# Performance work log

Hardware: AMD Instinct MI355X
Metric: run time of the kernel (lower is better)

## Reference

```python
import jax, jax.numpy as jnp
import numpy as np

N = 50000   # vertices
E = 25000   # hyperedges
NNZ = 400000  # incidence pairs (v, e)
D_IN = 512
D_OUT = 512  # heads * out_channels, heads=1


def setup_inputs() -> dict:
    key = jax.random.key(0)
    kx, kw, kv, ke = jax.random.split(key, 4)
    X = jax.random.normal(kx, (N, D_IN), dtype=jnp.float32)
    W = jax.random.normal(kw, (D_OUT, D_IN), dtype=jnp.float32) * 0.02  # nn.Linear weight [out,in]
    vidx = jax.random.randint(kv, (NNZ,), 0, N, dtype=jnp.int32)
    eidx = jax.random.randint(ke, (NNZ,), 0, E, dtype=jnp.int32)
    # degE = 1/|e| (hyperedge size), degV = 1/deg(v), as precomputed by hyperg
    ones = jnp.ones((NNZ,), dtype=jnp.float32)
    edge_sz = jax.ops.segment_sum(ones, eidx, num_segments=E)
    vert_dg = jax.ops.segment_sum(ones, vidx, num_segments=N)
    degE = 1.0 / jnp.maximum(edge_sz, 1.0)
    degV = 1.0 / jnp.maximum(vert_dg, 1.0)
    Wdiag = jnp.ones((E,), dtype=jnp.float32)
    return {"X": X, "W": W, "degE": degE, "degV": degV, "Wdiag": Wdiag,
            "vidx": vidx, "eidx": eidx}


def reference(X, W, degE, degV, Wdiag, vidx, eidx):
    # Dense projection: X @ W^T (nn.Linear, no bias)
    Xp = jnp.einsum('nd,od->no', X, W)                      # [N, D_OUT]
    # Stage 1: vertex -> hyperedge (first_aggr: mean via degE), weighted by Wdiag
    Xe = jax.ops.segment_sum(Xp[vidx], eidx, num_segments=E)  # [E, D_OUT]
    Xe = Xe * (degE * Wdiag)[:, None]
    # Stage 2: hyperedge -> vertex, normalized by degV
    Xv = jax.ops.segment_sum(Xe[eidx], vidx, num_segments=N)  # [N, D_OUT]
    Xv = Xv * degV[:, None]
    return Xv
```

## Files before the change

kernel.cpp:

```cpp
#include <hip/hip_runtime.h>

typedef unsigned short u16;
typedef unsigned int   u32;
typedef __attribute__((ext_vector_type(4))) float f32x4;
typedef __attribute__((ext_vector_type(4))) u32   u32x4;
typedef __attribute__((ext_vector_type(4))) int   i32x4;
typedef __attribute__((ext_vector_type(8))) __bf16 bf16x8;

constexpr int NV   = 50000;
constexpr int NE   = 25000;
constexpr int NNZp = 400000;
constexpr int D    = 512;
constexpr int MP2  = 25088;
constexpr int NBE  = 25;
constexpr int NBV  = 49;
constexpr int BPS1 = 391;
constexpr int BPS2 = 1563;

static __device__ __forceinline__ u16 f2bf(float f) {
  u32 u = __float_as_uint(f);
  u32 r = (u + 0x7fffu + ((u >> 16) & 1u)) >> 16;
  return (u16)r;
}
static __device__ __forceinline__ u32 pk2(float a, float b) {
  return (u32)f2bf(a) | ((u32)f2bf(b) << 16);
}

static __device__ __forceinline__ void gload_lds16(const u16* g, u16* l) {
  __builtin_amdgcn_global_load_lds(
      (const __attribute__((address_space(1))) u32*)g,
      (__attribute__((address_space(3))) u32*)l, 16, 0, 0);
}

__global__ void zero_kernel(int* cntE, int* cntV, int* dhistE, int* dhistV) {
  int i = blockIdx.x * 256 + threadIdx.x;
  if (i < NE) cntE[i] = 0;
  if (i < NV) cntV[i] = 0;
  if (i < 64) { dhistE[i] = 0; dhistV[i] = 0; }
}

__global__ void hist_kernel(const int* __restrict__ vidx, const int* __restrict__ eidx,
                            int* cntE, int* cntV) {
  int i = blockIdx.x * 256 + threadIdx.x;
  if (i < NNZp) {
    atomicAdd(&cntE[eidx[i]], 1);
    atomicAdd(&cntV[vidx[i]], 1);
  }
}

__global__ __launch_bounds__(256) void deghist_kernel(
    const int* __restrict__ cntE, const int* __restrict__ cntV, int* dhistE, int* dhistV) {
  __shared__ int lhE[64], lhV[64];
  int t = threadIdx.x;
  if (t < 64) { lhE[t] = 0; lhV[t] = 0; }
  __syncthreads();
  int i = blockIdx.x * 256 + t;
  if (i < NE) atomicAdd(&lhE[min(cntE[i], 63)], 1);
  if (i < NV) atomicAdd(&lhV[min(cntV[i], 63)], 1);
  __syncthreads();
  if (t < 64) { if (lhE[t]) atomicAdd(&dhistE[t], lhE[t]); }
  else if (t < 128) { int u = t - 64; if (lhV[u]) atomicAdd(&dhistV[u], lhV[u]); }
}

__global__ __launch_bounds__(256) void scan1_kernel(
    const int* __restrict__ cntE, const int* __restrict__ cntV,
    int* offE, int* offV, int* blkSum) {
  const bool isE = blockIdx.x < NBE;
  const int* cnt = isE ? cntE : cntV;
  int* off = isE ? offE : offV;
  const int len = isE ? NE : NV;
  const int t = threadIdx.x;
  const int base = (isE ? blockIdx.x : blockIdx.x - NBE) * 1024 + t * 4;
  int4 c = {0, 0, 0, 0};
  if (base + 4 <= len) c = *(const int4*)(cnt + base);
  else {
    if (base + 0 < len) c.x = cnt[base + 0];
    if (base + 1 < len) c.y = cnt[base + 1];
    if (base + 2 < len) c.z = cnt[base + 2];
    if (base + 3 < len) c.w = cnt[base + 3];
  }
  int s = c.x + c.y + c.z + c.w;
  __shared__ int sm[256];
  sm[t] = s;
  __syncthreads();
  for (int d = 1; d < 256; d <<= 1) {
    int u = (t >= d) ? sm[t - d] : 0;
    __syncthreads();
    sm[t] += u;
    __syncthreads();
  }
  int ex = sm[t] - s;
  int4 o;
  o.x = ex; o.y = o.x + c.x; o.z = o.y + c.y; o.w = o.z + c.z;
  if (base + 4 <= len) *(int4*)(off + base) = o;
  else {
    if (base + 0 < len) off[base + 0] = o.x;
    if (base + 1 < len) off[base + 1] = o.y;
    if (base + 2 < len) off[base + 2] = o.z;
    if (base + 3 < len) off[base + 3] = o.w;
  }
  if (t == 255) blkSum[blockIdx.x] = sm[255];
}

__global__ void scan2_kernel(int* blkSum, const int* __restrict__ dhistE,
                             const int* __restrict__ dhistV, int* dcurE, int* dcurV) {
  int wv = threadIdx.x >> 6, lane = threadIdx.x & 63;
  const int* s; int* d; int len;
  if (wv == 0)      { s = blkSum;       d = blkSum;       len = NBE; }
  else if (wv == 1) { s = blkSum + NBE; d = blkSum + NBE; len = NBV; }
  else if (wv == 2) { s = dhistE;       d = dcurE;        len = 64;  }
  else              { s = dhistV;       d = dcurV;        len = 64;  }
  int v = (lane < len) ? s[lane] : 0;
  int incl = v;
#pragma unroll
  for (int dd = 1; dd < 64; dd <<= 1) {
    int u = __shfl_up(incl, dd, 64);
    if (lane >= dd) incl += u;
  }
  if (lane < len) d[lane] = incl - v;
}

__global__ __launch_bounds__(256) void scan3_kernel(
    int* offE, int* offV, int* curE, int* curV, const int* __restrict__ blkSum) {
  const bool isE = blockIdx.x < NBE;
  int* off = isE ? offE : offV;
  int* cur = isE ? curE : curV;
  const int len = isE ? NE : NV;
  const int pref = blkSum[blockIdx.x];
  const int base = (isE ? blockIdx.x : blockIdx.x - NBE) * 1024 + threadIdx.x * 4;
  if (base + 4 <= len) {
    int4 o = *(int4*)(off + base);
    o.x += pref; o.y += pref; o.z += pref; o.w += pref;
    *(int4*)(off + base) = o;
    *(int4*)(cur + base) = o;
  } else {
    for (int q = 0; q < 4; q++)
      if (base + q < len) { int v = off[base + q] + pref; off[base + q] = v; cur[base + q] = v; }
  }
}

__global__ void scatter_kernel(const int* __restrict__ vidx, const int* __restrict__ eidx,
                               int* curE, int* curV, int* csr_ev, int* csr_ve) {
  int i = blockIdx.x * 256 + threadIdx.x;
  if (i < NNZp) {
    int e = eidx[i], v = vidx[i];
    csr_ev[atomicAdd(&curE[e], 1)] = v;
    csr_ve[atomicAdd(&curV[v], 1)] = e;
  }
}

__global__ __launch_bounds__(256) void degsort_kernel(
    const int* __restrict__ cntE, const int* __restrict__ offE,
    const int* __restrict__ cntV, const int* __restrict__ offV,
    const float* __restrict__ degV, int* dcurE, int* dcurV,
    i32x4* sE_meta, i32x4* sV_meta) {
  __shared__ int lhE[64], lhV[64], lbE[64], lbV[64];
  int t = threadIdx.x;
  if (t < 64) { lhE[t] = 0; lhV[t] = 0; }
  __syncthreads();
  int i = blockIdx.x * 256 + t;
  int bE = 0, rE = 0, bV = 0, rV = 0;
  if (i < NE) { bE = min(cntE[i], 63); rE = atomicAdd(&lhE[bE], 1); }
  if (i < NV) { bV = min(cntV[i], 63); rV = atomicAdd(&lhV[bV], 1); }
  __syncthreads();
  if (t < 64) { lbE[t] = lhE[t] ? atomicAdd(&dcurE[t], lhE[t]) : 0; }
  else if (t < 128) { int u = t - 64; lbV[u] = lhV[u] ? atomicAdd(&dcurV[u], lhV[u]) : 0; }
  __syncthreads();
  if (i < NE) {
    int r = lbE[bE] + rE;
    i32x4 m = { i, offE[i], cntE[i], 0 };
    sE_meta[r] = m;
  }
  if (i < NV) {
    int r = lbV[bV] + rV;
    i32x4 m = { i, offV[i], cntV[i], __float_as_int(degV[i]) };
    sV_meta[r] = m;
  }
}

__global__ __launch_bounds__(256) void convert_kernel(
    const float* __restrict__ X, const float* __restrict__ W,
    u16* __restrict__ Xb, u16* __restrict__ Wb) {
  constexpr size_t NX = (size_t)NV * D;
  size_t i = ((size_t)blockIdx.x * 256 + threadIdx.x) * 8;
  const float* src;
  u16* dst;
  if (i < NX) {
    int n = (int)(i >> 9);
    int col = (int)(i & 511);
    int t = col >> 5, w = col & 31;
    src = X + i;
    dst = Xb + (size_t)t * NV * 32 + (size_t)n * 32 + w;
  } else {
    src = W + (i - NX);
    dst = Wb + (i - NX);
  }
  f32x4 a = *(const f32x4*)src;
  f32x4 b = *(const f32x4*)(src + 4);
  u32x4 p = { pk2(a[0], a[1]), pk2(a[2], a[3]), pk2(b[0], b[1]), pk2(b[2], b[3]) };
  __builtin_nontemporal_store(p, (u32x4*)dst);
}

__global__ __launch_bounds__(256) void stage1_kernel(
    const u16* __restrict__ Xb, const i32x4* __restrict__ sE_meta,
    const int* __restrict__ csr_ev, u16* __restrict__ XeR) {
  const int wave = threadIdx.x >> 6;
  const int lane = threadIdx.x & 63;
  const int g    = lane >> 2;
  const int c    = lane & 3;
  const int bid  = blockIdx.x;
  const int xcd  = bid & 7;
  const int tmp  = bid >> 3;
  const int phase = (tmp >= BPS1) ? 1 : 0;
  const int eg    = tmp - phase * BPS1;
  const int t     = xcd + 8 * phase;
  const int rank  = eg * 64 + wave * 16 + g;
  const u16* base = Xb + (size_t)t * NV * 32;
  int e = 0, start = 0, cnt = 0;
  if (rank < NE) {
    i32x4 m = __builtin_nontemporal_load(sE_meta + rank);
    e = m.x; start = m.y; cnt = m.z;
  }
  float acc[8] = {};
  int b0 = 0;
  for (; b0 + 16 <= cnt; b0 += 16) {
    int idx[16];
#pragma unroll
    for (int p = 0; p < 16; p++) idx[p] = __builtin_nontemporal_load(csr_ev + start + b0 + p);
    u32x4 pk[16];
#pragma unroll
    for (int p = 0; p < 16; p++) pk[p] = *(const u32x4*)(base + (size_t)idx[p] * 32 + c * 8);
#pragma unroll
    for (int p = 0; p < 16; p++)
#pragma unroll
      for (int q = 0; q < 4; q++) {
        u32 u = pk[p][q];
        acc[2 * q]     += __uint_as_float(u << 16);
        acc[2 * q + 1] += __uint_as_float(u & 0xffff0000u);
      }
  }
  const int rem = cnt - b0;
  if (rem > 0) {
    int idx[16];
#pragma unroll
    for (int p = 0; p < 16; p++) {
      int j = __builtin_nontemporal_load(csr_ev + start + b0 + p);
      idx[p] = (p < rem) ? j : 0;
    }
    u32x4 pk[16];
#pragma unroll
    for (int p = 0; p < 16; p++) pk[p] = *(const u32x4*)(base + (size_t)idx[p] * 32 + c * 8);
#pragma unroll
    for (int p = 0; p < 16; p++)
      if (p < rem)
#pragma unroll
        for (int q = 0; q < 4; q++) {
          u32 u = pk[p][q];
          acc[2 * q]     += __uint_as_float(u << 16);
          acc[2 * q + 1] += __uint_as_float(u & 0xffff0000u);
        }
  }
  if (rank < NE) {
    u32x4 o = { pk2(acc[0], acc[1]), pk2(acc[2], acc[3]),
                pk2(acc[4], acc[5]), pk2(acc[6], acc[7]) };
    __builtin_nontemporal_store(o, (u32x4*)(XeR + (size_t)e * D + t * 32 + c * 8));
  }
}

__global__ __launch_bounds__(256) void gemm_kernel(const u16* __restrict__ A,
                                                   const u16* __restrict__ B,
                                                   const float* __restrict__ degE,
                                                   const float* __restrict__ Wdiag,
                                                   u16* __restrict__ C) {
  __shared__ u16 sA[128 * 32];
  __shared__ u16 sB[128 * 32];
  const int tid  = threadIdx.x;
  const int lane = tid & 63;
  const int wave = tid >> 6;
  const int bm = blockIdx.y * 128;
  const int bn = blockIdx.x * 128;
  const int wm = (wave >> 1) * 64;
  const int wn = (wave & 1) * 64;
  const int lr = lane & 15;
  const int lk = (lane >> 4) * 8;
  const int srow = lane >> 2;
  const int scol = (lane & 3) * 8;

  f32x4 acc[4][4] = {};

  for (int kt = 0; kt < D; kt += 32) {
    __syncthreads();
#pragma unroll
    for (int c = 0; c < 2; c++) {
      const int ar = wave * 16 + c * 64;
      gload_lds16(A + (size_t)(bm + ar + srow) * D + kt + scol, &sA[ar * 32]);
      gload_lds16(B + (size_t)(bn + ar + srow) * D + kt + scol, &sB[ar * 32]);
    }
    __syncthreads();

    bf16x8 af[4], bfr[4];
#pragma unroll
    for (int i = 0; i < 4; i++) af[i]  = *(const bf16x8*)&sA[(wm + i * 16 + lr) * 32 + lk];
#pragma unroll
    for (int j = 0; j < 4; j++) bfr[j] = *(const bf16x8*)&sB[(wn + j * 16 + lr) * 32 + lk];
#pragma unroll
    for (int i = 0; i < 4; i++)
#pragma unroll
      for (int j = 0; j < 4; j++)
        acc[i][j] = __builtin_amdgcn_mfma_f32_16x16x32_bf16(af[i], bfr[j], acc[i][j], 0, 0, 0);
  }

#pragma unroll
  for (int i = 0; i < 4; i++)
#pragma unroll
    for (int r = 0; r < 4; r++) {
      int row = bm + wm + i * 16 + (lane >> 4) * 4 + r;
      if (row < NE) {
        float se = degE[row] * Wdiag[row];
#pragma unroll
        for (int j = 0; j < 4; j++) {
          int col = bn + wn + lr + j * 16;
          int s = col >> 6, w = col & 63;
          __builtin_nontemporal_store(f2bf(acc[i][j][r] * se),
                                      C + (size_t)s * MP2 * 64 + (size_t)row * 64 + w);
        }
      }
    }
}

__global__ __launch_bounds__(256) void stage2_kernel(
    const u16* __restrict__ Xe2, const i32x4* __restrict__ sV_meta,
    const int* __restrict__ csr_ve, float* __restrict__ out) {
  const int wave = threadIdx.x >> 6;
  const int lane = threadIdx.x & 63;
  const int g    = lane >> 3;
  const int c    = lane & 7;
  const int s    = blockIdx.x & 7;
  const int vg   = blockIdx.x >> 3;
  const int rank = vg * 32 + wave * 8 + g;
  const u16* base = Xe2 + (size_t)s * MP2 * 64;
  int v = 0, start = 0, cnt = 0;
  float dv = 0.f;
  if (rank < NV) {
    i32x4 m = __builtin_nontemporal_load(sV_meta + rank);
    v = m.x; start = m.y; cnt = m.z; dv = __int_as_float(m.w);
  }
  float acc[8] = {};
  int b0 = 0;
  for (; b0 + 16 <= cnt; b0 += 16) {
    int idx[16];
#pragma unroll
    for (int p = 0; p < 16; p++) idx[p] = __builtin_nontemporal_load(csr_ve + start + b0 + p);
    u32x4 pk[16];
#pragma unroll
    for (int p = 0; p < 16; p++) pk[p] = *(const u32x4*)(base + (size_t)idx[p] * 64 + c * 8);
#pragma unroll
    for (int p = 0; p < 16; p++)
#pragma unroll
      for (int q = 0; q < 4; q++) {
        u32 u = pk[p][q];
        acc[2 * q]     += __uint_as_float(u << 16);
        acc[2 * q + 1] += __uint_as_float(u & 0xffff0000u);
      }
  }
  const int rem = cnt - b0;
  if (rem > 0) {
    int idx[16];
#pragma unroll
    for (int p = 0; p < 16; p++) {
      int j = __builtin_nontemporal_load(csr_ve + start + b0 + p);
      idx[p] = (p < rem) ? j : 0;
    }
    u32x4 pk[16];
#pragma unroll
    for (int p = 0; p < 16; p++) pk[p] = *(const u32x4*)(base + (size_t)idx[p] * 64 + c * 8);
#pragma unroll
    for (int p = 0; p < 16; p++)
      if (p < rem)
#pragma unroll
        for (int q = 0; q < 4; q++) {
          u32 u = pk[p][q];
          acc[2 * q]     += __uint_as_float(u << 16);
          acc[2 * q + 1] += __uint_as_float(u & 0xffff0000u);
        }
  }
  if (rank < NV) {
    float* orow = out + (size_t)v * D + s * 64 + c * 8;
    f32x4 o0 = { acc[0] * dv, acc[1] * dv, acc[2] * dv, acc[3] * dv };
    f32x4 o1 = { acc[4] * dv, acc[5] * dv, acc[6] * dv, acc[7] * dv };
    __builtin_nontemporal_store(o0, (f32x4*)orow);
    __builtin_nontemporal_store(o1, (f32x4*)(orow + 4));
  }
}

extern "C" void kernel_launch(void* const* d_in, const int* in_sizes, int n_in,
                              void* d_out, int out_size, void* d_ws, size_t ws_size,
                              hipStream_t stream) {
  const float* X     = (const float*)d_in[0];
  const float* W     = (const float*)d_in[1];
  const float* degE  = (const float*)d_in[2];
  const float* degV  = (const float*)d_in[3];
  const float* Wdiag = (const float*)d_in[4];
  const int*   vidx  = (const int*)d_in[5];
  const int*   eidx  = (const int*)d_in[6];
  float* out = (float*)d_out;

  char* p = (char*)d_ws;
  auto take = [&](size_t bytes) { char* r = p; p += (bytes + 255) & ~(size_t)255; return r; };
  u16* Xb     = (u16*)take((size_t)NV * D * 2);
  u16* Wb     = (u16*)take((size_t)D * D * 2);
  u16* XeR    = (u16*)take((size_t)MP2 * D * 2);
  u16* Xe2    = (u16*)take((size_t)MP2 * D * 2);
  int* cntE   = (int*)take((size_t)NE * 4);
  int* offE   = (int*)take((size_t)NE * 4);
  int* curE   = (int*)take((size_t)NE * 4);
  int* cntV   = (int*)take((size_t)NV * 4);
  int* offV   = (int*)take((size_t)NV * 4);
  int* curV   = (int*)take((size_t)NV * 4);
  int* csr_ev = (int*)take((size_t)NNZp * 4);
  int* csr_ve = (int*)take((size_t)NNZp * 4);
  int* blkSum = (int*)take((size_t)(NBE + NBV) * 4);
  int* dhistE = (int*)take(64 * 4);
  int* dhistV = (int*)take(64 * 4);
  int* dcurE  = (int*)take(64 * 4);
  int* dcurV  = (int*)take(64 * 4);
  i32x4* sE_meta = (i32x4*)take((size_t)NE * 16);
  i32x4* sV_meta = (i32x4*)take((size_t)NV * 16);

  constexpr size_t NCONV = ((size_t)NV * D + (size_t)D * D) / 8 / 256;
  constexpr int NSEG = (NV + 255) / 256;

  zero_kernel   <<<NSEG, 256, 0, stream>>>(cntE, cntV, dhistE, dhistV);
  hist_kernel   <<<(NNZp + 255) / 256, 256, 0, stream>>>(vidx, eidx, cntE, cntV);
  deghist_kernel<<<NSEG, 256, 0, stream>>>(cntE, cntV, dhistE, dhistV);
  scan1_kernel  <<<NBE + NBV, 256, 0, stream>>>(cntE, cntV, offE, offV, blkSum);
  scan2_kernel  <<<1, 256, 0, stream>>>(blkSum, dhistE, dhistV, dcurE, dcurV);
  scan3_kernel  <<<NBE + NBV, 256, 0, stream>>>(offE, offV, curE, curV, blkSum);
  scatter_kernel<<<(NNZp + 255) / 256, 256, 0, stream>>>(vidx, eidx, curE, curV, csr_ev, csr_ve);
  degsort_kernel<<<NSEG, 256, 0, stream>>>(cntE, offE, cntV, offV, degV, dcurE, dcurV,
                                           sE_meta, sV_meta);
  convert_kernel<<<NCONV, 256, 0, stream>>>(X, W, Xb, Wb);
  stage1_kernel <<<BPS1 * 16, 256, 0, stream>>>(Xb, sE_meta, csr_ev, XeR);
  gemm_kernel   <<<dim3(D / 128, MP2 / 128), 256, 0, stream>>>(XeR, Wb, degE, Wdiag, Xe2);
  stage2_kernel <<<BPS2 * 8, 256, 0, stream>>>(Xe2, sV_meta, csr_ve, out);
}
```

Before: 527.1 us.

## Share gather indices via lane shuffles and drop nontemporal hints

The two gather kernels stop having every lane load all 16 indices of a batch. Each lane group now loads its indices cooperatively, one or two per lane, and broadcasts them with __shfl, in batches of 8 with per-element bounds checks. This replaces the 16-wide unrolled main loop and its separate remainder path. All nontemporal loads and stores become ordinary loads and stores, so written intermediates can stay in cache for the next kernel. The trade-off is less memory-level parallelism per iteration, since 8 gathers are in flight instead of 16, plus extra shuffle and branch overhead.

```diff
diff --git a/kernel.cpp b/kernel.cpp
--- a/kernel.cpp
+++ b/kernel.cpp
@@ -198,7 +198,7 @@
   f32x4 a = *(const f32x4*)src;
   f32x4 b = *(const f32x4*)(src + 4);
   u32x4 p = { pk2(a[0], a[1]), pk2(a[2], a[3]), pk2(b[0], b[1]), pk2(b[2], b[3]) };
-  __builtin_nontemporal_store(p, (u32x4*)dst);
+  *(u32x4*)dst = p;
 }
 
 __global__ __launch_bounds__(256) void stage1_kernel(
@@ -218,52 +218,38 @@
   const u16* base = Xb + (size_t)t * NV * 32;
   int e = 0, start = 0, cnt = 0;
   if (rank < NE) {
-    i32x4 m = __builtin_nontemporal_load(sE_meta + rank);
+    i32x4 m = sE_meta[rank];
     e = m.x; start = m.y; cnt = m.z;
   }
   float acc[8] = {};
-  int b0 = 0;
-  for (; b0 + 16 <= cnt; b0 += 16) {
-    int idx[16];
-#pragma unroll
-    for (int p = 0; p < 16; p++) idx[p] = __builtin_nontemporal_load(csr_ev + start + b0 + p);
-    u32x4 pk[16];
-#pragma unroll
-    for (int p = 0; p < 16; p++) pk[p] = *(const u32x4*)(base + (size_t)idx[p] * 32 + c * 8);
-#pragma unroll
-    for (int p = 0; p < 16; p++)
-#pragma unroll
-      for (int q = 0; q < 4; q++) {
-        u32 u = pk[p][q];
-        acc[2 * q]     += __uint_as_float(u << 16);
-        acc[2 * q + 1] += __uint_as_float(u & 0xffff0000u);
+  for (int j0 = 0; j0 < cnt; j0 += 8) {
+    int i0 = 0, i1 = 0;
+    if (j0 + c < cnt)     i0 = csr_ev[start + j0 + c];
+    if (j0 + 4 + c < cnt) i1 = csr_ev[start + j0 + 4 + c];
+    u32x4 pk[8];
+#pragma unroll
+    for (int k = 0; k < 8; k++) {
+      if (j0 + k < cnt) {
+        int v = __shfl((k < 4) ? i0 : i1, (lane & ~3) | (k & 3), 64);
+        pk[k] = *(const u32x4*)(base + (size_t)v * 32 + c * 8);
       }
-  }
-  const int rem = cnt - b0;
-  if (rem > 0) {
-    int idx[16];
-#pragma unroll
-    for (int p = 0; p < 16; p++) {
-      int j = __builtin_nontemporal_load(csr_ev + start + b0 + p);
-      idx[p] = (p < rem) ? j : 0;
-    }
-    u32x4 pk[16];
-#pragma unroll
-    for (int p = 0; p < 16; p++) pk[p] = *(const u32x4*)(base + (size_t)idx[p] * 32 + c * 8);
-#pragma unroll
-    for (int p = 0; p < 16; p++)
-      if (p < rem)
+    }
+#pragma unroll
+    for (int k = 0; k < 8; k++) {
+      if (j0 + k < cnt) {
 #pragma unroll
         for (int q = 0; q < 4; q++) {
-          u32 u = pk[p][q];
+          u32 u = pk[k][q];
           acc[2 * q]     += __uint_as_float(u << 16);
           acc[2 * q + 1] += __uint_as_float(u & 0xffff0000u);
         }
+      }
+    }
   }
   if (rank < NE) {
     u32x4 o = { pk2(acc[0], acc[1]), pk2(acc[2], acc[3]),
                 pk2(acc[4], acc[5]), pk2(acc[6], acc[7]) };
-    __builtin_nontemporal_store(o, (u32x4*)(XeR + (size_t)e * D + t * 32 + c * 8));
+    *(u32x4*)(XeR + (size_t)e * D + t * 32 + c * 8) = o;
   }
 }
 
@@ -321,8 +307,7 @@
         for (int j = 0; j < 4; j++) {
           int col = bn + wn + lr + j * 16;
           int s = col >> 6, w = col & 63;
-          __builtin_nontemporal_store(f2bf(acc[i][j][r] * se),
-                                      C + (size_t)s * MP2 * 64 + (size_t)row * 64 + w);
+          C[(size_t)s * MP2 * 64 + (size_t)row * 64 + w] = f2bf(acc[i][j][r] * se);
         }
       }
     }
@@ -342,54 +327,39 @@
   int v = 0, start = 0, cnt = 0;
   float dv = 0.f;
   if (rank < NV) {
-    i32x4 m = __builtin_nontemporal_load(sV_meta + rank);
+    i32x4 m = sV_meta[rank];
     v = m.x; start = m.y; cnt = m.z; dv = __int_as_float(m.w);
   }
   float acc[8] = {};
-  int b0 = 0;
-  for (; b0 + 16 <= cnt; b0 += 16) {
-    int idx[16];
-#pragma unroll
-    for (int p = 0; p < 16; p++) idx[p] = __builtin_nontemporal_load(csr_ve + start + b0 + p);
-    u32x4 pk[16];
-#pragma unroll
-    for (int p = 0; p < 16; p++) pk[p] = *(const u32x4*)(base + (size_t)idx[p] * 64 + c * 8);
-#pragma unroll
-    for (int p = 0; p < 16; p++)
-#pragma unroll
-      for (int q = 0; q < 4; q++) {
-        u32 u = pk[p][q];
-        acc[2 * q]     += __uint_as_float(u << 16);
-        acc[2 * q + 1] += __uint_as_float(u & 0xffff0000u);
+  for (int j0 = 0; j0 < cnt; j0 += 8) {
+    int i0 = 0;
+    if (j0 + c < cnt) i0 = csr_ve[start + j0 + c];
+    u32x4 pk[8];
+#pragma unroll
+    for (int k = 0; k < 8; k++) {
+      if (j0 + k < cnt) {
+        int e = __shfl(i0, (lane & ~7) | k, 64);
+        pk[k] = *(const u32x4*)(base + (size_t)e * 64 + c * 8);
       }
-  }
-  const int rem = cnt - b0;
-  if (rem > 0) {
-    int idx[16];
-#pragma unroll
-    for (int p = 0; p < 16; p++) {
-      int j = __builtin_nontemporal_load(csr_ve + start + b0 + p);
-      idx[p] = (p < rem) ? j : 0;
-    }
-    u32x4 pk[16];
-#pragma unroll
-    for (int p = 0; p < 16; p++) pk[p] = *(const u32x4*)(base + (size_t)idx[p] * 64 + c * 8);
-#pragma unroll
-    for (int p = 0; p < 16; p++)
-      if (p < rem)
+    }
+#pragma unroll
+    for (int k = 0; k < 8; k++) {
+      if (j0 + k < cnt) {
 #pragma unroll
         for (int q = 0; q < 4; q++) {
-          u32 u = pk[p][q];
+          u32 u = pk[k][q];
           acc[2 * q]     += __uint_as_float(u << 16);
           acc[2 * q + 1] += __uint_as_float(u & 0xffff0000u);
         }
+      }
+    }
   }
   if (rank < NV) {
     float* orow = out + (size_t)v * D + s * 64 + c * 8;
     f32x4 o0 = { acc[0] * dv, acc[1] * dv, acc[2] * dv, acc[3] * dv };
     f32x4 o1 = { acc[4] * dv, acc[5] * dv, acc[6] * dv, acc[7] * dv };
-    __builtin_nontemporal_store(o0, (f32x4*)orow);
-    __builtin_nontemporal_store(o1, (f32x4*)(orow + 4));
+    *(f32x4*)orow = o0;
+    *(f32x4*)(orow + 4) = o1;
   }
 }
 
```

Measured after the change: 422.3 us. 1.25x faster.

## Fuse degree histogram and degree sort into scan kernels, shuffle-distribute gather indices

Applied to the files above, without the earlier changes.

Removes the separate deghist and degsort kernels by folding the degree histogram into scan1 and the bucketed meta placement into scan3, cutting two launches and extra passes over the count arrays. In stage1 and stage2 the lanes of each group now load distinct CSR indices and broadcast them with wave shuffles, instead of every lane loading all 16 indices. Nontemporal loads on meta and index arrays become plain loads. Degree-sorted order within a bucket changes, which only affects scheduling.

```diff
diff --git a/kernel.cpp b/kernel.cpp
--- a/kernel.cpp
+++ b/kernel.cpp
@@ -48,26 +48,13 @@
   }
 }
 
-__global__ __launch_bounds__(256) void deghist_kernel(
-    const int* __restrict__ cntE, const int* __restrict__ cntV, int* dhistE, int* dhistV) {
-  __shared__ int lhE[64], lhV[64];
-  int t = threadIdx.x;
-  if (t < 64) { lhE[t] = 0; lhV[t] = 0; }
-  __syncthreads();
-  int i = blockIdx.x * 256 + t;
-  if (i < NE) atomicAdd(&lhE[min(cntE[i], 63)], 1);
-  if (i < NV) atomicAdd(&lhV[min(cntV[i], 63)], 1);
-  __syncthreads();
-  if (t < 64) { if (lhE[t]) atomicAdd(&dhistE[t], lhE[t]); }
-  else if (t < 128) { int u = t - 64; if (lhV[u]) atomicAdd(&dhistV[u], lhV[u]); }
-}
-
 __global__ __launch_bounds__(256) void scan1_kernel(
     const int* __restrict__ cntE, const int* __restrict__ cntV,
-    int* offE, int* offV, int* blkSum) {
+    int* offE, int* offV, int* blkSum, int* dhistE, int* dhistV) {
   const bool isE = blockIdx.x < NBE;
   const int* cnt = isE ? cntE : cntV;
   int* off = isE ? offE : offV;
+  int* dhist = isE ? dhistE : dhistV;
   const int len = isE ? NE : NV;
   const int t = threadIdx.x;
   const int base = (isE ? blockIdx.x : blockIdx.x - NBE) * 1024 + t * 4;
@@ -81,8 +68,14 @@
   }
   int s = c.x + c.y + c.z + c.w;
   __shared__ int sm[256];
+  __shared__ int lh[64];
+  if (t < 64) lh[t] = 0;
   sm[t] = s;
   __syncthreads();
+  if (base + 0 < len) atomicAdd(&lh[min(c.x, 63)], 1);
+  if (base + 1 < len) atomicAdd(&lh[min(c.y, 63)], 1);
+  if (base + 2 < len) atomicAdd(&lh[min(c.z, 63)], 1);
+  if (base + 3 < len) atomicAdd(&lh[min(c.w, 63)], 1);
   for (int d = 1; d < 256; d <<= 1) {
     int u = (t >= d) ? sm[t - d] : 0;
     __syncthreads();
@@ -100,6 +93,7 @@
     if (base + 3 < len) off[base + 3] = o.w;
   }
   if (t == 255) blkSum[blockIdx.x] = sm[255];
+  if (t < 64 && lh[t]) atomicAdd(&dhist[t], lh[t]);
 }
 
 __global__ void scan2_kernel(int* blkSum, const int* __restrict__ dhistE,
@@ -121,22 +115,57 @@
 }
 
 __global__ __launch_bounds__(256) void scan3_kernel(
-    int* offE, int* offV, int* curE, int* curV, const int* __restrict__ blkSum) {
+    int* offE, int* offV, int* curE, int* curV, const int* __restrict__ blkSum,
+    const int* __restrict__ cntE, const int* __restrict__ cntV,
+    const float* __restrict__ degV, int* dcurE, int* dcurV,
+    i32x4* sE_meta, i32x4* sV_meta) {
   const bool isE = blockIdx.x < NBE;
   int* off = isE ? offE : offV;
   int* cur = isE ? curE : curV;
+  const int* cnt = isE ? cntE : cntV;
+  int* dcur = isE ? dcurE : dcurV;
+  i32x4* meta = isE ? sE_meta : sV_meta;
   const int len = isE ? NE : NV;
   const int pref = blkSum[blockIdx.x];
-  const int base = (isE ? blockIdx.x : blockIdx.x - NBE) * 1024 + threadIdx.x * 4;
+  const int t = threadIdx.x;
+  const int base = (isE ? blockIdx.x : blockIdx.x - NBE) * 1024 + t * 4;
+  __shared__ int lh[64], lb[64];
+  if (t < 64) lh[t] = 0;
+  __syncthreads();
+  int os[4] = {}, cs[4] = {};
+  bool val[4] = {};
   if (base + 4 <= len) {
     int4 o = *(int4*)(off + base);
-    o.x += pref; o.y += pref; o.z += pref; o.w += pref;
-    *(int4*)(off + base) = o;
-    *(int4*)(cur + base) = o;
+    int4 c = *(const int4*)(cnt + base);
+    os[0] = o.x + pref; os[1] = o.y + pref; os[2] = o.z + pref; os[3] = o.w + pref;
+    cs[0] = c.x; cs[1] = c.y; cs[2] = c.z; cs[3] = c.w;
+    val[0] = val[1] = val[2] = val[3] = true;
+    int4 oo = {os[0], os[1], os[2], os[3]};
+    *(int4*)(off + base) = oo;
+    *(int4*)(cur + base) = oo;
   } else {
     for (int q = 0; q < 4; q++)
-      if (base + q < len) { int v = off[base + q] + pref; off[base + q] = v; cur[base + q] = v; }
-  }
+      if (base + q < len) {
+        os[q] = off[base + q] + pref; cs[q] = cnt[base + q]; val[q] = true;
+        off[base + q] = os[q]; cur[base + q] = os[q];
+      }
+  }
+  int bq[4] = {}, rk[4] = {};
+#pragma unroll
+  for (int q = 0; q < 4; q++)
+    if (val[q]) { bq[q] = min(cs[q], 63); rk[q] = atomicAdd(&lh[bq[q]], 1); }
+  __syncthreads();
+  if (t < 64) lb[t] = lh[t] ? atomicAdd(&dcur[t], lh[t]) : 0;
+  __syncthreads();
+#pragma unroll
+  for (int q = 0; q < 4; q++)
+    if (val[q]) {
+      int id = base + q;
+      int dw = 0;
+      if (!isE) dw = __float_as_int(degV[id]);
+      i32x4 m = { id, os[q], cs[q], dw };
+      meta[lb[bq[q]] + rk[q]] = m;
+    }
 }
 
 __global__ void scatter_kernel(const int* __restrict__ vidx, const int* __restrict__ eidx,
@@ -146,35 +175,6 @@
     int e = eidx[i], v = vidx[i];
     csr_ev[atomicAdd(&curE[e], 1)] = v;
     csr_ve[atomicAdd(&curV[v], 1)] = e;
-  }
-}
-
-__global__ __launch_bounds__(256) void degsort_kernel(
-    const int* __restrict__ cntE, const int* __restrict__ offE,
-    const int* __restrict__ cntV, const int* __restrict__ offV,
-    const float* __restrict__ degV, int* dcurE, int* dcurV,
-    i32x4* sE_meta, i32x4* sV_meta) {
-  __shared__ int lhE[64], lhV[64], lbE[64], lbV[64];
-  int t = threadIdx.x;
-  if (t < 64) { lhE[t] = 0; lhV[t] = 0; }
-  __syncthreads();
-  int i = blockIdx.x * 256 + t;
-  int bE = 0, rE = 0, bV = 0, rV = 0;
-  if (i < NE) { bE = min(cntE[i], 63); rE = atomicAdd(&lhE[bE], 1); }
-  if (i < NV) { bV = min(cntV[i], 63); rV = atomicAdd(&lhV[bV], 1); }
-  __syncthreads();
-  if (t < 64) { lbE[t] = lhE[t] ? atomicAdd(&dcurE[t], lhE[t]) : 0; }
-  else if (t < 128) { int u = t - 64; lbV[u] = lhV[u] ? atomicAdd(&dcurV[u], lhV[u]) : 0; }
-  __syncthreads();
-  if (i < NE) {
-    int r = lbE[bE] + rE;
-    i32x4 m = { i, offE[i], cntE[i], 0 };
-    sE_meta[r] = m;
-  }
-  if (i < NV) {
-    int r = lbV[bV] + rV;
-    i32x4 m = { i, offV[i], cntV[i], __float_as_int(degV[i]) };
-    sV_meta[r] = m;
   }
 }
 
@@ -218,44 +218,53 @@
   const u16* base = Xb + (size_t)t * NV * 32;
   int e = 0, start = 0, cnt = 0;
   if (rank < NE) {
-    i32x4 m = __builtin_nontemporal_load(sE_meta + rank);
+    i32x4 m = sE_meta[rank];
     e = m.x; start = m.y; cnt = m.z;
   }
   float acc[8] = {};
-  int b0 = 0;
-  for (; b0 + 16 <= cnt; b0 += 16) {
-    int idx[16];
-#pragma unroll
-    for (int p = 0; p < 16; p++) idx[p] = __builtin_nontemporal_load(csr_ev + start + b0 + p);
+  int j0 = 0;
+  for (; j0 + 16 <= cnt; j0 += 16) {
+    int ia = csr_ev[start + j0 + c];
+    int ib = csr_ev[start + j0 + 4 + c];
+    int ic = csr_ev[start + j0 + 8 + c];
+    int id = csr_ev[start + j0 + 12 + c];
     u32x4 pk[16];
 #pragma unroll
-    for (int p = 0; p < 16; p++) pk[p] = *(const u32x4*)(base + (size_t)idx[p] * 32 + c * 8);
-#pragma unroll
-    for (int p = 0; p < 16; p++)
+    for (int k = 0; k < 16; k++) {
+      int src = (k < 4) ? ia : (k < 8) ? ib : (k < 12) ? ic : id;
+      int v = __shfl(src, (lane & ~3) | (k & 3), 64);
+      pk[k] = *(const u32x4*)(base + (size_t)v * 32 + c * 8);
+    }
+#pragma unroll
+    for (int k = 0; k < 16; k++)
 #pragma unroll
       for (int q = 0; q < 4; q++) {
-        u32 u = pk[p][q];
+        u32 u = pk[k][q];
         acc[2 * q]     += __uint_as_float(u << 16);
         acc[2 * q + 1] += __uint_as_float(u & 0xffff0000u);
       }
   }
-  const int rem = cnt - b0;
-  if (rem > 0) {
-    int idx[16];
-#pragma unroll
-    for (int p = 0; p < 16; p++) {
-      int j = __builtin_nontemporal_load(csr_ev + start + b0 + p);
-      idx[p] = (p < rem) ? j : 0;
-    }
+  const int rem = cnt - j0;
+  if (rem) {
+    int ia = csr_ev[start + j0 + c];
+    int ib = csr_ev[start + j0 + 4 + c];
+    int ic = csr_ev[start + j0 + 8 + c];
+    int id = csr_ev[start + j0 + 12 + c];
     u32x4 pk[16];
 #pragma unroll
-    for (int p = 0; p < 16; p++) pk[p] = *(const u32x4*)(base + (size_t)idx[p] * 32 + c * 8);
-#pragma unroll
-    for (int p = 0; p < 16; p++)
-      if (p < rem)
+    for (int k = 0; k < 16; k++) {
+      if (k < rem) {
+        int src = (k < 4) ? ia : (k < 8) ? ib : (k < 12) ? ic : id;
+        int v = __shfl(src, (lane & ~3) | (k & 3), 64);
+        pk[k] = *(const u32x4*)(base + (size_t)v * 32 + c * 8);
+      }
+    }
+#pragma unroll
+    for (int k = 0; k < 16; k++)
+      if (k < rem)
 #pragma unroll
         for (int q = 0; q < 4; q++) {
-          u32 u = pk[p][q];
+          u32 u = pk[k][q];
           acc[2 * q]     += __uint_as_float(u << 16);
           acc[2 * q + 1] += __uint_as_float(u & 0xffff0000u);
         }
@@ -342,44 +351,47 @@
   int v = 0, start = 0, cnt = 0;
   float dv = 0.f;
   if (rank < NV) {
-    i32x4 m = __builtin_nontemporal_load(sV_meta + rank);
+    i32x4 m = sV_meta[rank];
     v = m.x; start = m.y; cnt = m.z; dv = __int_as_float(m.w);
   }
   float acc[8] = {};
-  int b0 = 0;
-  for (; b0 + 16 <= cnt; b0 += 16) {
-    int idx[16];
-#pragma unroll
-    for (int p = 0; p < 16; p++) idx[p] = __builtin_nontemporal_load(csr_ve + start + b0 + p);
+  int j0 = 0;
+  for (; j0 + 16 <= cnt; j0 += 16) {
+    int ia = csr_ve[start + j0 + c];
+    int ib = csr_ve[start + j0 + 8 + c];
     u32x4 pk[16];
 #pragma unroll
-    for (int p = 0; p < 16; p++) pk[p] = *(const u32x4*)(base + (size_t)idx[p] * 64 + c * 8);
-#pragma unroll
-    for (int p = 0; p < 16; p++)
+    for (int k = 0; k < 16; k++) {
+      int e = __shfl((k < 8) ? ia : ib, (lane & ~7) | (k & 7), 64);
+      pk[k] = *(const u32x4*)(base + (size_t)e * 64 + c * 8);
+    }
+#pragma unroll
+    for (int k = 0; k < 16; k++)
 #pragma unroll
       for (int q = 0; q < 4; q++) {
-        u32 u = pk[p][q];
+        u32 u = pk[k][q];
         acc[2 * q]     += __uint_as_float(u << 16);
         acc[2 * q + 1] += __uint_as_float(u & 0xffff0000u);
       }
   }
-  const int rem = cnt - b0;
-  if (rem > 0) {
-    int idx[16];
-#pragma unroll
-    for (int p = 0; p < 16; p++) {
-      int j = __builtin_nontemporal_load(csr_ve + start + b0 + p);
-      idx[p] = (p < rem) ? j : 0;
-    }
+  const int rem = cnt - j0;
+  if (rem) {
+    int ia = csr_ve[start + j0 + c];
+    int ib = csr_ve[start + j0 + 8 + c];
     u32x4 pk[16];
 #pragma unroll
-    for (int p = 0; p < 16; p++) pk[p] = *(const u32x4*)(base + (size_t)idx[p] * 64 + c * 8);
-#pragma unroll
-    for (int p = 0; p < 16; p++)
-      if (p < rem)
+    for (int k = 0; k < 16; k++) {
+      if (k < rem) {
+        int e = __shfl((k < 8) ? ia : ib, (lane & ~7) | (k & 7), 64);
+        pk[k] = *(const u32x4*)(base + (size_t)e * 64 + c * 8);
+      }
+    }
+#pragma unroll
+    for (int k = 0; k < 16; k++)
+      if (k < rem)
 #pragma unroll
         for (int q = 0; q < 4; q++) {
-          u32 u = pk[p][q];
+          u32 u = pk[k][q];
           acc[2 * q]     += __uint_as_float(u << 16);
           acc[2 * q + 1] += __uint_as_float(u & 0xffff0000u);
         }
@@ -432,13 +444,12 @@
 
   zero_kernel   <<<NSEG, 256, 0, stream>>>(cntE, cntV, dhistE, dhistV);
   hist_kernel   <<<(NNZp + 255) / 256, 256, 0, stream>>>(vidx, eidx, cntE, cntV);
-  deghist_kernel<<<NSEG, 256, 0, stream>>>(cntE, cntV, dhistE, dhistV);
-  scan1_kernel  <<<NBE + NBV, 256, 0, stream>>>(cntE, cntV, offE, offV, blkSum);
+  scan1_kernel  <<<NBE + NBV, 256, 0, stream>>>(cntE, cntV, offE, offV, blkSum, dhistE, dhistV);
   scan2_kernel  <<<1, 256, 0, stream>>>(blkSum, dhistE, dhistV, dcurE, dcurV);
-  scan3_kernel  <<<NBE + NBV, 256, 0, stream>>>(offE, offV, curE, curV, blkSum);
+  scan3_kernel  <<<NBE + NBV, 256, 0, stream>>>(offE, offV, curE, curV, blkSum,
+                                                cntE, cntV, degV, dcurE, dcurV,
+                                                sE_meta, sV_meta);
   scatter_kernel<<<(NNZp + 255) / 256, 256, 0, stream>>>(vidx, eidx, curE, curV, csr_ev, csr_ve);
-  degsort_kernel<<<NSEG, 256, 0, stream>>>(cntE, offE, cntV, offV, degV, dcurE, dcurV,
-                                           sE_meta, sV_meta);
   convert_kernel<<<NCONV, 256, 0, stream>>>(X, W, Xb, Wb);
   stage1_kernel <<<BPS1 * 16, 256, 0, stream>>>(Xb, sE_meta, csr_ev, XeR);
   gemm_kernel   <<<dim3(D / 128, MP2 / 128), 256, 0, stream>>>(XeR, Wb, degE, Wdiag, Xe2);
```

Result: faster. 435.3 us (-17.4%).
